# Kernel tuning notes

Hardware: AMD Instinct MI355X
Metric: run time of the kernel (lower is better)

## Reference

```python
import jax, jax.numpy as jnp
import numpy as np

EMBED = 128
HEADS = 8
HEAD_DIM = EMBED // HEADS

def setup_inputs() -> dict:
    key = jax.random.key(0)
    ks = jax.random.split(key, 8)
    B, N = 2, 4096
    values = jax.random.normal(ks[0], (B, N, EMBED), dtype=jnp.float32)
    keys = jax.random.normal(ks[1], (B, N, EMBED), dtype=jnp.float32)
    query = jax.random.normal(ks[2], (B, N, EMBED), dtype=jnp.float32)
    s = 1.0 / np.sqrt(HEAD_DIM)
    Wv = jax.random.normal(ks[3], (HEAD_DIM, HEAD_DIM), dtype=jnp.float32) * s
    Wk = jax.random.normal(ks[4], (HEAD_DIM, HEAD_DIM), dtype=jnp.float32) * s
    Wq = jax.random.normal(ks[5], (HEAD_DIM, HEAD_DIM), dtype=jnp.float32) * s
    Wo = jax.random.normal(ks[6], (EMBED, EMBED), dtype=jnp.float32) * (1.0 / np.sqrt(EMBED))
    bo = jnp.zeros((EMBED,), dtype=jnp.float32)
    return {"values": values, "keys": keys, "query": query,
            "Wv": Wv, "Wk": Wk, "Wq": Wq, "Wo": Wo, "bo": bo}

def reference(values, keys, query, Wv, Wk, Wq, Wo, bo):
    B, N, _ = query.shape
    # split heads: [B,N,H,Dh]
    v = values.reshape(B, N, HEADS, HEAD_DIM)
    k = keys.reshape(B, N, HEADS, HEAD_DIM)
    q = query.reshape(B, N, HEADS, HEAD_DIM)
    # per-head linear (torch Linear: x @ W.T), same weight for all heads
    v = jnp.einsum('bnhd,ed->bnhe', v, Wv)
    k = jnp.einsum('bnhd,ed->bnhe', k, Wk)
    q = jnp.einsum('bnhd,ed->bnhe', q, Wq)
    # scores [B,H,N,N], note scale by sqrt(embed_size) as in original
    energy = jnp.einsum('bqhd,bkhd->bhqk', q, k) / jnp.sqrt(jnp.float32(EMBED))
    attn = jax.nn.softmax(energy, axis=-1)
    out = jnp.einsum('bhql,blhd->bqhd', attn, v).reshape(B, N, EMBED)
    return out @ Wo.T + bo
```

## Files before the change

### kernel.cpp

```cpp
#include <hip/hip_runtime.h>

#define BB 2
#define NN 4096
#define HH 8
#define DD 16
#define EE 128
#define LBLK 128
#define NTH 16

typedef _Float16 f16;
typedef _Float16 f16x4 __attribute__((ext_vector_type(4)));
typedef _Float16 f16x2 __attribute__((ext_vector_type(2)));
typedef _Float16 f16x8 __attribute__((ext_vector_type(8)));
typedef __fp16 h16x2 __attribute__((ext_vector_type(2)));
typedef float f32x4 __attribute__((ext_vector_type(4)));

#define QSCALE 0.12751741f

__global__ __launch_bounds__(256) void proj_kernel(
    const float* __restrict__ vals, const float* __restrict__ keys,
    const float* __restrict__ query,
    const float* __restrict__ Wv, const float* __restrict__ Wk,
    const float* __restrict__ Wq, const float* __restrict__ Wo,
    f16* __restrict__ Qp, f16* __restrict__ Kp, f16* __restrict__ Vt,
    f16* __restrict__ Wo16)
{
    if (blockIdx.x >= 768) {
        const int i = (blockIdx.x - 768) * 256 + threadIdx.x;
        Wo16[i] = (f16)Wo[i];
        return;
    }
    __shared__ float W[256];
    const int p = blockIdx.x >> 8;
    const float* Wsrc = (p == 0) ? Wv : ((p == 1) ? Wk : Wq);
    W[threadIdx.x] = Wsrc[threadIdx.x];
    __syncthreads();

    const int idx = ((blockIdx.x & 255) << 8) | threadIdx.x;
    const int n = idx & 4095;
    const int h = (idx >> 12) & 7;
    const int b = idx >> 15;

    const float* xsrc = (p == 0) ? vals : ((p == 1) ? keys : query);
    const float4* xp = (const float4*)(xsrc + (size_t)(b * NN + n) * EE + h * DD);
    const float4 x0 = xp[0], x1 = xp[1], x2 = xp[2], x3 = xp[3];
    const float scale = (p == 2) ? QSCALE : 1.0f;

    alignas(16) f16 out[16];
    #pragma unroll
    for (int e = 0; e < 16; e++) {
        const float4* wr = (const float4*)(W + e * 16);
        const float4 w0 = wr[0], w1 = wr[1], w2 = wr[2], w3 = wr[3];
        float acc = x0.x * w0.x + x0.y * w0.y + x0.z * w0.z + x0.w * w0.w
                  + x1.x * w1.x + x1.y * w1.y + x1.z * w1.z + x1.w * w1.w
                  + x2.x * w2.x + x2.y * w2.y + x2.z * w2.z + x2.w * w2.w
                  + x3.x * w3.x + x3.y * w3.y + x3.z * w3.z + x3.w * w3.w;
        out[e] = (f16)(acc * scale);
    }

    if (p == 0) {
        f16* dst = Vt + (size_t)(b * HH + h) * DD * NN + n;
        #pragma unroll
        for (int e = 0; e < 16; e++) dst[(size_t)e * NN] = out[e];
    } else {
        f16* dst = ((p == 1) ? Kp : Qp) + (size_t)((b * HH + h) * NN + n) * DD;
        ((uint4*)dst)[0] = ((const uint4*)out)[0];
        ((uint4*)dst)[1] = ((const uint4*)out)[1];
    }
}

__global__ __launch_bounds__(256, 8) void attn_kernel(
    const f16* __restrict__ Qp, const f16* __restrict__ Kp,
    const f16* __restrict__ Vt, float* __restrict__ Oacc,
    float* __restrict__ den)
{
    __shared__ alignas(16) f16 Kl[2][2048];
    __shared__ alignas(16) f16 Vl[2][2048];

    const int tid = threadIdx.x;
    const int lane = tid & 63;
    const int wave = tid >> 6;
    const int r = lane & 15;
    const int g = lane >> 4;

    const int bid = blockIdx.x;
    const int half = bid & 1;
    const int qt = (bid >> 1) & 63;
    const int bh = bid >> 7;
    const int q0 = qt * 64 + wave * 16;
    const int L0 = half * (NN / 2);

    const bool isK = tid < 128;
    const f16* gbase;
    int w0, w1;
    size_t gstep;
    if (isK) {
        const int spair = tid >> 6;
        const int lp = tid & 63;
        const int rr = lp & 15, gg = lp >> 4;
        const int lam = 8 * (rr >> 2) + (rr & 3);
        gbase = Kp + ((size_t)bh * NN + L0 + 64 * spair + lam) * DD + 4 * gg;
        gstep = (size_t)LBLK * DD;
        w0 = (2 * spair) * 512 + lp * 8;
        w1 = (2 * spair + 1) * 512 + lp * 8;
    } else {
        const int v = tid - 128;
        const int s = v >> 5;
        const int rr = v & 15;
        const int gp = (v >> 4) & 1;
        gbase = Vt + ((size_t)bh * DD + rr) * NN + L0 + 32 * s + 16 * gp;
        gstep = (size_t)LBLK;
        w0 = s * 512 + rr * 32 + gp * 16;
        w1 = w0 + 8;
    }

    const f16x4 qf = *(const f16x4*)(Qp + ((size_t)bh * NN + q0 + r) * DD + 4 * g);

    f16x8 sA, sB;
#define STAGE_LOAD() { \
    if (isK) { \
        const f16x4 a0 = *(const f16x4*)(gbase + 0); \
        const f16x4 a1 = *(const f16x4*)(gbase + 64); \
        const f16x4 a2 = *(const f16x4*)(gbase + 512); \
        const f16x4 a3 = *(const f16x4*)(gbase + 576); \
        sA = __builtin_shufflevector(a0, a1, 0,1,2,3,4,5,6,7); \
        sB = __builtin_shufflevector(a2, a3, 0,1,2,3,4,5,6,7); \
    } else { \
        sA = *(const f16x8*)(gbase + 0); \
        sB = *(const f16x8*)(gbase + 8); \
    } \
    gbase += gstep; }

    STAGE_LOAD();
    {
        f16* wp = isK ? &Kl[0][0] : &Vl[0][0];
        *(f16x8*)(wp + w0) = sA;
        *(f16x8*)(wp + w1) = sB;
    }
    __syncthreads();

    f32x4 acc0 = {0.f,0.f,0.f,0.f}, acc1 = {0.f,0.f,0.f,0.f};
    float da = 0.f, db = 0.f;
    const h16x2 ones = {(__fp16)1.0f, (__fp16)1.0f};
    int cur = 0;

    for (int t = 0; t < NTH; ++t) {
        if (t < NTH - 1) STAGE_LOAD();

        const f16* Kb = &Kl[cur][0];
        const f16* Vb = &Vl[cur][0];
        #pragma unroll
        for (int s = 0; s < 4; ++s) {
            const f16x8 kf8 = *(const f16x8*)(Kb + s * 512 + lane * 8);
            const f16x8 vf8 = *(const f16x8*)(Vb + s * 512 + r * 32 + g * 8);
            const f16x4 kfA = __builtin_shufflevector(kf8, kf8, 0, 1, 2, 3);
            const f16x4 kfB = __builtin_shufflevector(kf8, kf8, 4, 5, 6, 7);
            const f32x4 z = {0.f, 0.f, 0.f, 0.f};
            const f32x4 st0 = __builtin_amdgcn_mfma_f32_16x16x16f16(kfA, qf, z, 0, 0, 0);
            const f32x4 st1 = __builtin_amdgcn_mfma_f32_16x16x16f16(kfB, qf, z, 0, 0, 0);
            const float e0 = __builtin_amdgcn_exp2f(st0[0]);
            const float e1 = __builtin_amdgcn_exp2f(st0[1]);
            const float e2 = __builtin_amdgcn_exp2f(st0[2]);
            const float e3 = __builtin_amdgcn_exp2f(st0[3]);
            const float f0 = __builtin_amdgcn_exp2f(st1[0]);
            const float f1 = __builtin_amdgcn_exp2f(st1[1]);
            const float f2 = __builtin_amdgcn_exp2f(st1[2]);
            const float f3 = __builtin_amdgcn_exp2f(st1[3]);
            const h16x2 h0 = __builtin_amdgcn_cvt_pkrtz(e0, e1);
            const h16x2 h1 = __builtin_amdgcn_cvt_pkrtz(e2, e3);
            const h16x2 h2 = __builtin_amdgcn_cvt_pkrtz(f0, f1);
            const h16x2 h3 = __builtin_amdgcn_cvt_pkrtz(f2, f3);
            if (s & 1) {
                db = __builtin_amdgcn_fdot2(h0, ones, db, false);
                db = __builtin_amdgcn_fdot2(h1, ones, db, false);
                db = __builtin_amdgcn_fdot2(h2, ones, db, false);
                db = __builtin_amdgcn_fdot2(h3, ones, db, false);
            } else {
                da = __builtin_amdgcn_fdot2(h0, ones, da, false);
                da = __builtin_amdgcn_fdot2(h1, ones, da, false);
                da = __builtin_amdgcn_fdot2(h2, ones, da, false);
                da = __builtin_amdgcn_fdot2(h3, ones, da, false);
            }
            const f16x4 pA = __builtin_shufflevector(
                __builtin_bit_cast(f16x2, h0), __builtin_bit_cast(f16x2, h1), 0, 1, 2, 3);
            const f16x4 pB = __builtin_shufflevector(
                __builtin_bit_cast(f16x2, h2), __builtin_bit_cast(f16x2, h3), 0, 1, 2, 3);
            const f16x8 pf8 = __builtin_shufflevector(pA, pB, 0, 1, 2, 3, 4, 5, 6, 7);
            if (s & 1) {
                acc1 = __builtin_amdgcn_mfma_f32_16x16x32_f16(vf8, pf8, acc1, 0, 0, 0);
            } else {
                acc0 = __builtin_amdgcn_mfma_f32_16x16x32_f16(vf8, pf8, acc0, 0, 0, 0);
            }
        }

        if (t < NTH - 1) {
            f16* wp = (isK ? &Kl[cur ^ 1][0] : &Vl[cur ^ 1][0]);
            *(f16x8*)(wp + w0) = sA;
            *(f16x8*)(wp + w1) = sB;
        }
        __syncthreads();
        cur ^= 1;
    }
#undef STAGE_LOAD

    float dt = da + db;
    dt += __shfl_xor(dt, 16, 64);
    dt += __shfl_xor(dt, 32, 64);
    const f32x4 acc = acc0 + acc1;

    const int b = bh >> 3, h = bh & 7;
    float* OaccH = Oacc + (size_t)half * (BB * NN * EE);
    *(f32x4*)(OaccH + ((size_t)(b * NN + q0 + r)) * EE + h * DD + 4 * g) = acc;
    if (lane < 16) {
        den[(size_t)(half * 16 + bh) * NN + q0 + lane] = dt;
    }
}

__global__ __launch_bounds__(256) void outproj_kernel(
    const float* __restrict__ Oacc, const float* __restrict__ den,
    const f16* __restrict__ Wo16, const float* __restrict__ bo,
    float* __restrict__ out)
{
    const int lane = threadIdx.x & 63;
    const int wave = threadIdx.x >> 6;
    const int r = lane & 15;
    const int g = lane >> 4;
    const int n0 = (blockIdx.x * 2 + (wave >> 1)) * 16;
    const int eh = (wave & 1) * 4;

    const int n = n0 + r;
    const int b = n >> 12;
    const int nn = n & 4095;
    const float* Oa0 = Oacc + (size_t)n * EE;
    const float* Oa1 = Oacc + (size_t)(BB * NN * EE) + (size_t)n * EE;

    f32x4 acc[4];
    #pragma unroll
    for (int e = 0; e < 4; e++) acc[e] = (f32x4){0.f, 0.f, 0.f, 0.f};

    #pragma unroll
    for (int k0 = 0; k0 < 8; k0++) {
        const size_t didx = (size_t)(b * 8 + k0) * NN + nn;
        const float inv = 1.0f / (den[didx] + den[(size_t)16 * NN + didx]);
        const f32x4 xa = *(const f32x4*)(Oa0 + k0 * 16 + 4 * g);
        const f32x4 xb = *(const f32x4*)(Oa1 + k0 * 16 + 4 * g);
        const float s0 = (xa[0] + xb[0]) * inv;
        const float s1 = (xa[1] + xb[1]) * inv;
        const float s2 = (xa[2] + xb[2]) * inv;
        const float s3 = (xa[3] + xb[3]) * inv;
        const f16x4 a = __builtin_shufflevector(
            __builtin_bit_cast(f16x2, __builtin_amdgcn_cvt_pkrtz(s0, s1)),
            __builtin_bit_cast(f16x2, __builtin_amdgcn_cvt_pkrtz(s2, s3)), 0, 1, 2, 3);
        #pragma unroll
        for (int e = 0; e < 4; e++) {
            const f16x4 bf = *(const f16x4*)(Wo16 + (size_t)((eh + e) * 16 + r) * EE + k0 * 16 + 4 * g);
            acc[e] = __builtin_amdgcn_mfma_f32_16x16x16f16(a, bf, acc[e], 0, 0, 0);
        }
    }

    #pragma unroll
    for (int e = 0; e < 4; e++) {
        const float bias = bo[(eh + e) * 16 + r];
        #pragma unroll
        for (int i = 0; i < 4; i++) {
            out[(size_t)(n0 + 4 * g + i) * EE + (eh + e) * 16 + r] = acc[e][i] + bias;
        }
    }
}

extern "C" void kernel_launch(void* const* d_in, const int* in_sizes, int n_in,
                              void* d_out, int out_size, void* d_ws, size_t ws_size,
                              hipStream_t stream)
{
    const float* vals  = (const float*)d_in[0];
    const float* keys  = (const float*)d_in[1];
    const float* query = (const float*)d_in[2];
    const float* Wv    = (const float*)d_in[3];
    const float* Wk    = (const float*)d_in[4];
    const float* Wq    = (const float*)d_in[5];
    const float* Wo    = (const float*)d_in[6];
    const float* bo    = (const float*)d_in[7];
    float* out = (float*)d_out;

    char* w = (char*)d_ws;
    f16*   Qp   = (f16*)(w);
    f16*   Kp   = (f16*)(w + (2u << 20));
    f16*   Vt   = (f16*)(w + (4u << 20));
    f16*   Wo16 = (f16*)(w + (6u << 20));
    float* den  = (float*)(w + (6u << 20) + 65536);
    float* Oacc = (float*)(w + (7u << 20));

    hipLaunchKernelGGL(proj_kernel, dim3(832), dim3(256), 0, stream,
                       vals, keys, query, Wv, Wk, Wq, Wo, Qp, Kp, Vt, Wo16);
    hipLaunchKernelGGL(attn_kernel, dim3(2048), dim3(256), 0, stream,
                       Qp, Kp, Vt, Oacc, den);
    hipLaunchKernelGGL(outproj_kernel, dim3(256), dim3(256), 0, stream,
                       Oacc, den, Wo16, bo, out);
}
```

Baseline: 59.54 us.

## Process two query tiles per wave to reuse K/V shared-memory loads

Each wave now handles 32 queries (two 16-row MFMA tiles) instead of 16, so every K and V fragment read from LDS feeds two score/PV computations, and the grid is halved. The V staging layout in shared memory changes so each lane reads a contiguous 8-element vector by lane index. The aim is to cut global and LDS traffic per query and the block count, at the cost of more registers (launch bound lowered to 4 blocks per CU) and less parallelism across blocks.

Result: no change. 59.10 us (-0.7%).

```diff
diff --git a/kernel.cpp b/kernel.cpp
--- a/kernel.cpp
+++ b/kernel.cpp
@@ -69,7 +69,7 @@
     }
 }
 
-__global__ __launch_bounds__(256, 8) void attn_kernel(
+__global__ __launch_bounds__(256, 4) void attn_kernel(
     const f16* __restrict__ Qp, const f16* __restrict__ Kp,
     const f16* __restrict__ Vt, float* __restrict__ Oacc,
     float* __restrict__ den)
@@ -85,9 +85,9 @@
 
     const int bid = blockIdx.x;
     const int half = bid & 1;
-    const int qt = (bid >> 1) & 63;
-    const int bh = bid >> 7;
-    const int q0 = qt * 64 + wave * 16;
+    const int qt = (bid >> 1) & 31;
+    const int bh = bid >> 6;
+    const int q0 = qt * 128 + wave * 32;
     const int L0 = half * (NN / 2);
 
     const bool isK = tid < 128;
@@ -105,16 +105,14 @@
         w1 = (2 * spair + 1) * 512 + lp * 8;
     } else {
         const int v = tid - 128;
-        const int s = v >> 5;
-        const int rr = v & 15;
-        const int gp = (v >> 4) & 1;
-        gbase = Vt + ((size_t)bh * DD + rr) * NN + L0 + 32 * s + 16 * gp;
+        gbase = Vt + ((size_t)bh * DD + (v & 15)) * NN + L0 + 32 * (v >> 6) + 8 * ((v >> 4) & 3);
         gstep = (size_t)LBLK;
-        w0 = s * 512 + rr * 32 + gp * 16;
-        w1 = w0 + 8;
-    }
-
-    const f16x4 qf = *(const f16x4*)(Qp + ((size_t)bh * NN + q0 + r) * DD + 4 * g);
+        w0 = v * 8;
+        w1 = 1024 + v * 8;
+    }
+
+    const f16x4 qf0 = *(const f16x4*)(Qp + ((size_t)bh * NN + q0 + r) * DD + 4 * g);
+    const f16x4 qf1 = *(const f16x4*)(Qp + ((size_t)bh * NN + q0 + 16 + r) * DD + 4 * g);
 
     f16x8 sA, sB;
 #define STAGE_LOAD() { \
@@ -127,7 +125,7 @@
         sB = __builtin_shufflevector(a2, a3, 0,1,2,3,4,5,6,7); \
     } else { \
         sA = *(const f16x8*)(gbase + 0); \
-        sB = *(const f16x8*)(gbase + 8); \
+        sB = *(const f16x8*)(gbase + 64); \
     } \
     gbase += gstep; }
 
@@ -140,10 +138,37 @@
     __syncthreads();
 
     f32x4 acc0 = {0.f,0.f,0.f,0.f}, acc1 = {0.f,0.f,0.f,0.f};
-    float da = 0.f, db = 0.f;
+    float da0 = 0.f, db0 = 0.f, da1 = 0.f, db1 = 0.f;
     const h16x2 ones = {(__fp16)1.0f, (__fp16)1.0f};
     int cur = 0;
 
+#define PROCESS(QF, ACC, DA, DB) { \
+    const f32x4 z = {0.f,0.f,0.f,0.f}; \
+    const f32x4 st0 = __builtin_amdgcn_mfma_f32_16x16x16f16(kfA, (QF), z, 0, 0, 0); \
+    const f32x4 st1 = __builtin_amdgcn_mfma_f32_16x16x16f16(kfB, (QF), z, 0, 0, 0); \
+    const float e0 = __builtin_amdgcn_exp2f(st0[0]); \
+    const float e1 = __builtin_amdgcn_exp2f(st0[1]); \
+    const float e2 = __builtin_amdgcn_exp2f(st0[2]); \
+    const float e3 = __builtin_amdgcn_exp2f(st0[3]); \
+    const float f0 = __builtin_amdgcn_exp2f(st1[0]); \
+    const float f1 = __builtin_amdgcn_exp2f(st1[1]); \
+    const float f2 = __builtin_amdgcn_exp2f(st1[2]); \
+    const float f3 = __builtin_amdgcn_exp2f(st1[3]); \
+    const h16x2 h0 = __builtin_amdgcn_cvt_pkrtz(e0, e1); \
+    const h16x2 h1 = __builtin_amdgcn_cvt_pkrtz(e2, e3); \
+    const h16x2 h2 = __builtin_amdgcn_cvt_pkrtz(f0, f1); \
+    const h16x2 h3 = __builtin_amdgcn_cvt_pkrtz(f2, f3); \
+    DA = __builtin_amdgcn_fdot2(h0, ones, DA, false); \
+    DA = __builtin_amdgcn_fdot2(h1, ones, DA, false); \
+    DB = __builtin_amdgcn_fdot2(h2, ones, DB, false); \
+    DB = __builtin_amdgcn_fdot2(h3, ones, DB, false); \
+    const f16x4 pA = __builtin_shufflevector( \
+        __builtin_bit_cast(f16x2, h0), __builtin_bit_cast(f16x2, h1), 0, 1, 2, 3); \
+    const f16x4 pB = __builtin_shufflevector( \
+        __builtin_bit_cast(f16x2, h2), __builtin_bit_cast(f16x2, h3), 0, 1, 2, 3); \
+    const f16x8 pf8 = __builtin_shufflevector(pA, pB, 0, 1, 2, 3, 4, 5, 6, 7); \
+    ACC = __builtin_amdgcn_mfma_f32_16x16x32_f16(vf8, pf8, ACC, 0, 0, 0); }
+
     for (int t = 0; t < NTH; ++t) {
         if (t < NTH - 1) STAGE_LOAD();
 
@@ -152,45 +177,11 @@
         #pragma unroll
         for (int s = 0; s < 4; ++s) {
             const f16x8 kf8 = *(const f16x8*)(Kb + s * 512 + lane * 8);
-            const f16x8 vf8 = *(const f16x8*)(Vb + s * 512 + r * 32 + g * 8);
+            const f16x8 vf8 = *(const f16x8*)(Vb + s * 512 + lane * 8);
             const f16x4 kfA = __builtin_shufflevector(kf8, kf8, 0, 1, 2, 3);
             const f16x4 kfB = __builtin_shufflevector(kf8, kf8, 4, 5, 6, 7);
-            const f32x4 z = {0.f, 0.f, 0.f, 0.f};
-            const f32x4 st0 = __builtin_amdgcn_mfma_f32_16x16x16f16(kfA, qf, z, 0, 0, 0);
-            const f32x4 st1 = __builtin_amdgcn_mfma_f32_16x16x16f16(kfB, qf, z, 0, 0, 0);
-            const float e0 = __builtin_amdgcn_exp2f(st0[0]);
-            const float e1 = __builtin_amdgcn_exp2f(st0[1]);
-            const float e2 = __builtin_amdgcn_exp2f(st0[2]);
-            const float e3 = __builtin_amdgcn_exp2f(st0[3]);
-            const float f0 = __builtin_amdgcn_exp2f(st1[0]);
-            const float f1 = __builtin_amdgcn_exp2f(st1[1]);
-            const float f2 = __builtin_amdgcn_exp2f(st1[2]);
-            const float f3 = __builtin_amdgcn_exp2f(st1[3]);
-            const h16x2 h0 = __builtin_amdgcn_cvt_pkrtz(e0, e1);
-            const h16x2 h1 = __builtin_amdgcn_cvt_pkrtz(e2, e3);
-            const h16x2 h2 = __builtin_amdgcn_cvt_pkrtz(f0, f1);
-            const h16x2 h3 = __builtin_amdgcn_cvt_pkrtz(f2, f3);
-            if (s & 1) {
-                db = __builtin_amdgcn_fdot2(h0, ones, db, false);
-                db = __builtin_amdgcn_fdot2(h1, ones, db, false);
-                db = __builtin_amdgcn_fdot2(h2, ones, db, false);
-                db = __builtin_amdgcn_fdot2(h3, ones, db, false);
-            } else {
-                da = __builtin_amdgcn_fdot2(h0, ones, da, false);
-                da = __builtin_amdgcn_fdot2(h1, ones, da, false);
-                da = __builtin_amdgcn_fdot2(h2, ones, da, false);
-                da = __builtin_amdgcn_fdot2(h3, ones, da, false);
-            }
-            const f16x4 pA = __builtin_shufflevector(
-                __builtin_bit_cast(f16x2, h0), __builtin_bit_cast(f16x2, h1), 0, 1, 2, 3);
-            const f16x4 pB = __builtin_shufflevector(
-                __builtin_bit_cast(f16x2, h2), __builtin_bit_cast(f16x2, h3), 0, 1, 2, 3);
-            const f16x8 pf8 = __builtin_shufflevector(pA, pB, 0, 1, 2, 3, 4, 5, 6, 7);
-            if (s & 1) {
-                acc1 = __builtin_amdgcn_mfma_f32_16x16x32_f16(vf8, pf8, acc1, 0, 0, 0);
-            } else {
-                acc0 = __builtin_amdgcn_mfma_f32_16x16x32_f16(vf8, pf8, acc0, 0, 0, 0);
-            }
+            PROCESS(qf0, acc0, da0, db0)
+            PROCESS(qf1, acc1, da1, db1)
         }
 
         if (t < NTH - 1) {
@@ -201,18 +192,23 @@
         __syncthreads();
         cur ^= 1;
     }
+#undef PROCESS
 #undef STAGE_LOAD
 
-    float dt = da + db;
-    dt += __shfl_xor(dt, 16, 64);
-    dt += __shfl_xor(dt, 32, 64);
-    const f32x4 acc = acc0 + acc1;
+    float d0 = da0 + db0;
+    d0 += __shfl_xor(d0, 16, 64);
+    d0 += __shfl_xor(d0, 32, 64);
+    float d1 = da1 + db1;
+    d1 += __shfl_xor(d1, 16, 64);
+    d1 += __shfl_xor(d1, 32, 64);
 
     const int b = bh >> 3, h = bh & 7;
     float* OaccH = Oacc + (size_t)half * (BB * NN * EE);
-    *(f32x4*)(OaccH + ((size_t)(b * NN + q0 + r)) * EE + h * DD + 4 * g) = acc;
+    *(f32x4*)(OaccH + ((size_t)(b * NN + q0 + r)) * EE + h * DD + 4 * g) = acc0;
+    *(f32x4*)(OaccH + ((size_t)(b * NN + q0 + 16 + r)) * EE + h * DD + 4 * g) = acc1;
     if (lane < 16) {
-        den[(size_t)(half * 16 + bh) * NN + q0 + lane] = dt;
+        den[(size_t)(half * 16 + bh) * NN + q0 + lane] = d0;
+        den[(size_t)(half * 16 + bh) * NN + q0 + 16 + lane] = d1;
     }
 }
 
@@ -292,7 +288,7 @@
 
     hipLaunchKernelGGL(proj_kernel, dim3(832), dim3(256), 0, stream,
                        vals, keys, query, Wv, Wk, Wq, Wo, Qp, Kp, Vt, Wo16);
-    hipLaunchKernelGGL(attn_kernel, dim3(2048), dim3(256), 0, stream,
+    hipLaunchKernelGGL(attn_kernel, dim3(1024), dim3(256), 0, stream,
                        Qp, Kp, Vt, Oacc, den);
     hipLaunchKernelGGL(outproj_kernel, dim3(256), dim3(256), 0, stream,
                        Oacc, den, Wo16, bo, out);
```
